# Optimization experiments

Hardware: AMD Instinct MI355X
Metric: run time of the kernel (lower is better)

## Reference

```python
import jax, jax.numpy as jnp
import numpy as np

HIDDEN = 1024
INTER = 256
N_EXPERTS = 16
B, T = 4, 2048
NEG_INF = -1000000000.0


def setup_inputs() -> dict:
    key = jax.random.key(0)
    ks = jax.random.split(key, 5)
    hidden_states = jax.random.normal(ks[0], (B, T, HIDDEN), dtype=jnp.float32)
    sim_matrix = jax.random.normal(ks[1], (HIDDEN, N_EXPERTS), dtype=jnp.float32)
    threshold = jnp.zeros((1,), dtype=jnp.float32)
    # torch Linear weights: w1 [I, C], w2 [C, I]; store per-expert stacked in
    # matmul-friendly layout: w1 [E, C, I], w2 [E, I, C]
    w1 = jax.random.normal(ks[2], (N_EXPERTS, HIDDEN, INTER), dtype=jnp.float32) / np.sqrt(HIDDEN)
    w2 = jax.random.normal(ks[3], (N_EXPERTS, INTER, HIDDEN), dtype=jnp.float32) / np.sqrt(INTER)
    return {"hidden_states": hidden_states, "sim_matrix": sim_matrix,
            "threshold": threshold, "w1": w1, "w2": w2}


def _l2norm(x, axis):
    return x / jnp.maximum(jnp.linalg.norm(x, axis=axis, keepdims=True), 1e-12)


def reference(hidden_states, sim_matrix, threshold, w1, w2):
    Bq, Tq, C = hidden_states.shape
    x = hidden_states.reshape(-1, C)                      # [N, C]
    # gate
    scores = _l2norm(x, -1) @ _l2norm(sim_matrix, 0)      # [N, E]
    activated = scores > threshold
    k_per_token = activated.sum(axis=-1)                  # [N] int
    masked = jnp.where(activated, scores, NEG_INF)
    routing_weights = jax.nn.softmax(masked, axis=-1)     # [N, E]
    # dense all-expert FFN
    h = jax.nn.gelu(jnp.einsum('nc,eci->nei', x, w1), approximate=False)
    out = jnp.einsum('nei,eic->nec', h, w2)               # [N, E, C]
    final = jnp.einsum('nec,ne->nc', out, routing_weights)
    return final.reshape(Bq, Tq, C), scores, k_per_token
```

## Files before the change

### kernel.cpp

```cpp
#include <hip/hip_runtime.h>
#include <hip/hip_bf16.h>
#include <math.h>

#define NTOK 8192
#define HID  1024
#define ISZ  256
#define NEXP 16
#define NBIG 4096

typedef __attribute__((ext_vector_type(8))) short bf16x8;
typedef __attribute__((ext_vector_type(4))) float f32x4;

__device__ __forceinline__ unsigned short f2bf(float f) {
  unsigned u = __float_as_uint(f);
  u += 0x7fff + ((u >> 16) & 1);
  return (unsigned short)(u >> 16);
}

__device__ __forceinline__ void async16(void* l, const void* g) {
  __builtin_amdgcn_global_load_lds(
      (const __attribute__((address_space(1))) unsigned int*)g,
      (__attribute__((address_space(3))) unsigned int*)l, 16, 0, 0);
}

__global__ void simnorm_kernel(const float* __restrict__ sm, float* __restrict__ inv_smn) {
  __shared__ float red[16][17];
  int t = threadIdx.x;
  int e = t & 15, g = t >> 4;
  float ss = 0.f;
  for (int c = g; c < HID; c += 16) {
    float v = sm[c * NEXP + e];
    ss += v * v;
  }
  red[e][g] = ss;
  __syncthreads();
  if (t < 16) {
    float s = 0.f;
    #pragma unroll
    for (int i = 0; i < 16; i++) s += red[t][i];
    inv_smn[t] = 1.f / fmaxf(sqrtf(s), 1e-12f);
  }
}

__global__ __launch_bounds__(256)
void gate_kernel(const float* __restrict__ x, const float* __restrict__ sm,
                 const float* __restrict__ thr, const float* __restrict__ inv_smn,
                 float* __restrict__ scores_out, float* __restrict__ k_out,
                 float* __restrict__ rw_out, unsigned short* __restrict__ xb_out) {
  const int n = blockIdx.x;
  const int t = threadIdx.x;
  const int lane = t & 63, wave = t >> 6;
  const float* xr = x + (size_t)n * HID;

  float p[16];
  #pragma unroll
  for (int e = 0; e < 16; e++) p[e] = 0.f;
  float ss = 0.f;

  #pragma unroll
  for (int q = 0; q < 4; q++) {
    int c = t + q * 256;
    float v = xr[c];
    ss += v * v;
    xb_out[(size_t)n * HID + c] = f2bf(v);
    const float4* smr = (const float4*)(sm + (size_t)c * NEXP);
    float4 s0 = smr[0], s1 = smr[1], s2 = smr[2], s3 = smr[3];
    p[0] += v * s0.x;  p[1] += v * s0.y;  p[2] += v * s0.z;  p[3] += v * s0.w;
    p[4] += v * s1.x;  p[5] += v * s1.y;  p[6] += v * s1.z;  p[7] += v * s1.w;
    p[8] += v * s2.x;  p[9] += v * s2.y;  p[10] += v * s2.z; p[11] += v * s2.w;
    p[12] += v * s3.x; p[13] += v * s3.y; p[14] += v * s3.z; p[15] += v * s3.w;
  }

  #pragma unroll
  for (int off = 32; off > 0; off >>= 1) {
    ss += __shfl_down(ss, off, 64);
    #pragma unroll
    for (int e = 0; e < 16; e++) p[e] += __shfl_down(p[e], off, 64);
  }

  __shared__ float red[4][17];
  __shared__ float sc[16];
  if (lane == 0) {
    red[wave][0] = ss;
    #pragma unroll
    for (int e = 0; e < 16; e++) red[wave][1 + e] = p[e];
  }
  __syncthreads();

  if (t < 16) {
    float d = red[0][1 + t] + red[1][1 + t] + red[2][1 + t] + red[3][1 + t];
    float ssum = red[0][0] + red[1][0] + red[2][0] + red[3][0];
    float inv_x = 1.f / fmaxf(sqrtf(ssum), 1e-12f);
    float s = d * inv_x * inv_smn[t];
    scores_out[(size_t)n * 16 + t] = s;
    sc[t] = s;
  }
  __syncthreads();

  if (t < 16) {
    float thrv = thr[0];
    float s = sc[t];
    bool act = s > thrv;
    float m = act ? s : -INFINITY;
    int cnt = act ? 1 : 0;
    #pragma unroll
    for (int off = 8; off > 0; off >>= 1) {
      m = fmaxf(m, __shfl_xor(m, off, 16));
      cnt += __shfl_xor(cnt, off, 16);
    }
    float pv;
    if (cnt > 0) pv = act ? expf(s - m) : 0.f;
    else         pv = 1.f;
    float sum = pv;
    #pragma unroll
    for (int off = 8; off > 0; off >>= 1) sum += __shfl_xor(sum, off, 16);
    rw_out[(size_t)n * 16 + t] = pv / sum;
    if (t == 0) k_out[n] = (float)cnt;
  }
}

__global__ __launch_bounds__(256)
void transpose_cast_kernel(const float* __restrict__ src, unsigned short* __restrict__ dst,
                           int R, int C, int dstride, int e_src_stride, int e_dst_mult) {
  __shared__ float tile[32][33];
  const int e = blockIdx.z;
  const int r0 = blockIdx.y * 32, c0 = blockIdx.x * 32;
  const int tx = threadIdx.x & 31, ty = threadIdx.x >> 5;
  const float* s = src + (size_t)e * e_src_stride;
  #pragma unroll
  for (int q = 0; q < 4; q++) {
    int r = r0 + ty + q * 8;
    tile[ty + q * 8][tx] = s[(size_t)r * C + c0 + tx];
  }
  __syncthreads();
  unsigned short* d = dst + (size_t)e * e_dst_mult;
  #pragma unroll
  for (int q = 0; q < 4; q++) {
    int cc = c0 + ty + q * 8;
    int r  = r0 + tx;
    d[(size_t)cc * dstride + r] = f2bf(tile[tx][ty + q * 8]);
  }
}

#define PHASE(QM, QN, SU, WAIT_)                                                      \
  {                                                                                   \
    bf16x8 afr[4][2], bfr[2][2];                                                      \
    _Pragma("unroll")                                                                 \
    for (int ml = 0; ml < 4; ml++) {                                                  \
      afr[ml][0] = *(const bf16x8*)(bufA + (QM)*16384 + wmo + ml*2048 + lro + colk0); \
      afr[ml][1] = *(const bf16x8*)(bufA + (QM)*16384 + wmo + ml*2048 + lro + colk1); \
    }                                                                                 \
    _Pragma("unroll")                                                                 \
    for (int nl = 0; nl < 2; nl++) {                                                  \
      bfr[nl][0] = *(const bf16x8*)(bufB + (QN)*16384 + wno + nl*2048 + lro + colk0); \
      bfr[nl][1] = *(const bf16x8*)(bufB + (QN)*16384 + wno + nl*2048 + lro + colk1); \
    }                                                                                 \
    _Pragma("unroll")                                                                 \
    for (int i = 0; i < 2; i++) {                                                     \
      if ((SU) == 0) async16(ldsAn + o16[i],         Ag + (size_t)aRow[i]*K + kn + aCol[i]);        \
      if ((SU) == 1) async16(ldsBn + o16[i],         Bg + (size_t)bRow[i]*K + kn + bCol[i]);        \
      if ((SU) == 2) async16(ldsAn + 16384 + o16[i], Ag + (size_t)(aRow[i] + 64)*K + kn + aCol[i]); \
      if ((SU) == 3) async16(ldsBn + 16384 + o16[i], Bg + (size_t)(bRow[i] + 32)*K + kn + bCol[i]); \
    }                                                                                 \
    __builtin_amdgcn_sched_barrier(0);                                                \
    __builtin_amdgcn_s_barrier();                                                     \
    asm volatile("s_waitcnt lgkmcnt(0)" ::: "memory");                                \
    __builtin_amdgcn_sched_barrier(0);                                                \
    __builtin_amdgcn_s_setprio(1);                                                    \
    _Pragma("unroll")                                                                 \
    for (int ml = 0; ml < 4; ml++)                                                    \
      _Pragma("unroll")                                                               \
      for (int nl = 0; nl < 2; nl++) {                                                \
        acc[(QM)*4+ml][(QN)*2+nl] = __builtin_amdgcn_mfma_f32_16x16x32_bf16(          \
            afr[ml][0], bfr[nl][0], acc[(QM)*4+ml][(QN)*2+nl], 0, 0, 0);              \
        acc[(QM)*4+ml][(QN)*2+nl] = __builtin_amdgcn_mfma_f32_16x16x32_bf16(          \
            afr[ml][1], bfr[nl][1], acc[(QM)*4+ml][(QN)*2+nl], 0, 0, 0);              \
      }                                                                               \
    __builtin_amdgcn_s_setprio(0);                                                    \
    __builtin_amdgcn_sched_barrier(0);                                                \
    if (WAIT_) { asm volatile("s_waitcnt vmcnt(4)" ::: "memory"); }                   \
    __builtin_amdgcn_s_barrier();                                                     \
  }

template <int EPI, int K, int NBN>
__global__ __launch_bounds__(512, 2)
void gemm256(const unsigned short* __restrict__ A, const unsigned short* __restrict__ B,
             float* __restrict__ Cf, unsigned short* __restrict__ Cb,
             const float* __restrict__ rw) {
  __shared__ __align__(1024) char lds[131072];
  constexpr int NT = K / 64;
  const int tid = threadIdx.x;
  const int lane = tid & 63, wid = tid >> 6;
  const int wm = wid >> 2, wn = wid & 3;
  const int lr = lane & 15;

  const int nwg = gridDim.x;
  const int cpx = nwg >> 3;
  const int wg = (blockIdx.x & 7) * cpx + (blockIdx.x >> 3);
  const int bm = wg / NBN, bn = wg % NBN;

  const int swz = (lr & 7) << 4;
  const int colk0 = ((lane >> 4) * 16) ^ swz;
  const int colk1 = (64 + (lane >> 4) * 16) ^ swz;
  const int wmo = wm * 8192, wno = wn * 4096, lro = lr * 128;

  int aRow[2], aCol[2], bRow[2], bCol[2], o16[2];
  #pragma unroll
  for (int i = 0; i < 2; i++) {
    int o = (i * 512 + tid) * 16;
    o16[i] = o;
    { int wmb = o >> 13, ob = o & 8191, r = ob >> 7, cb = ob & 127;
      aRow[i] = wmb * 128 + r; aCol[i] = (cb ^ ((r & 7) << 4)) >> 1; }
    { int wnb = o >> 12, ob = o & 4095, r = ob >> 7, cb = ob & 127;
      bRow[i] = wnb * 64 + r; bCol[i] = (cb ^ ((r & 7) << 4)) >> 1; }
  }

  const unsigned short* Ag = A + (size_t)bm * 256 * K;
  const unsigned short* Bg = B + (size_t)bn * 256 * K;

  f32x4 acc[8][4];
  #pragma unroll
  for (int m = 0; m < 8; m++)
    #pragma unroll
    for (int n = 0; n < 4; n++) acc[m][n] = (f32x4){0.f, 0.f, 0.f, 0.f};

  #pragma unroll
  for (int i = 0; i < 2; i++) async16(lds + o16[i],                 Ag + (size_t)aRow[i] * K + aCol[i]);
  #pragma unroll
  for (int i = 0; i < 2; i++) async16(lds + 65536 + o16[i],         Bg + (size_t)bRow[i] * K + bCol[i]);
  #pragma unroll
  for (int i = 0; i < 2; i++) async16(lds + 16384 + o16[i],         Ag + (size_t)(aRow[i] + 64) * K + aCol[i]);
  #pragma unroll
  for (int i = 0; i < 2; i++) async16(lds + 65536 + 16384 + o16[i], Bg + (size_t)(bRow[i] + 32) * K + bCol[i]);
  asm volatile("s_waitcnt vmcnt(0)" ::: "memory");
  __builtin_amdgcn_s_barrier();

  #pragma unroll 1
  for (int t = 0; t < NT; t += 2) {
    {
      const char* bufA = lds;
      const char* bufB = lds + 65536;
      char* ldsAn = lds + 32768;
      char* ldsBn = lds + 65536 + 32768;
      const int kn = ((t + 1) & (NT - 1)) << 6;
      PHASE(0, 0, 0, 1)
      PHASE(1, 0, 1, 1)
      PHASE(0, 1, 2, 0)
      PHASE(1, 1, 3, 1)
    }
    {
      const char* bufA = lds + 32768;
      const char* bufB = lds + 65536 + 32768;
      char* ldsAn = lds;
      char* ldsBn = lds + 65536;
      const int kn = ((t + 2) & (NT - 1)) << 6;
      PHASE(0, 0, 0, 1)
      PHASE(1, 0, 1, 1)
      PHASE(0, 1, 2, 0)
      PHASE(1, 1, 3, 1)
    }
  }

  asm volatile("s_waitcnt vmcnt(0)" ::: "memory");

  const int jr = (lane >> 4) * 4;
  if (EPI == 1) {
    float wrow[8][4];
    #pragma unroll
    for (int m = 0; m < 8; m++)
      #pragma unroll
      for (int j = 0; j < 4; j++)
        wrow[m][j] = rw[(size_t)(bm * 256 + wm * 128 + m * 16 + jr + j) * 16 + bn];
    #pragma unroll
    for (int m = 0; m < 8; m++) {
      #pragma unroll
      for (int n = 0; n < 4; n++) {
        int col = bn * 256 + wn * 64 + n * 16 + lr;
        #pragma unroll
        for (int j = 0; j < 4; j++) {
          int r = bm * 256 + wm * 128 + m * 16 + jr + j;
          float v = acc[m][n][j];
          float g = 0.7978845608f * (v + 0.044715f * v * v * v);
          float e = __expf(2.f * g);
          float th = 1.f - 2.f / (e + 1.f);
          float ge = 0.5f * v * (1.f + th);
          Cb[(size_t)r * NBIG + col] = f2bf(ge * wrow[m][j]);
        }
      }
    }
  } else {
    #pragma unroll
    for (int m = 0; m < 8; m++) {
      #pragma unroll
      for (int n = 0; n < 4; n++) {
        int col = bn * 256 + wn * 64 + n * 16 + lr;
        #pragma unroll
        for (int j = 0; j < 4; j++) {
          int r = bm * 256 + wm * 128 + m * 16 + jr + j;
          Cf[(size_t)r * HID + col] = acc[m][n][j];
        }
      }
    }
  }
}

extern "C" void kernel_launch(void* const* d_in, const int* in_sizes, int n_in,
                              void* d_out, int out_size, void* d_ws, size_t ws_size,
                              hipStream_t stream) {
  const float* x   = (const float*)d_in[0];
  const float* sm  = (const float*)d_in[1];
  const float* thr = (const float*)d_in[2];
  const float* w1  = (const float*)d_in[3];
  const float* w2  = (const float*)d_in[4];

  float* out_final  = (float*)d_out;
  float* out_scores = out_final + (size_t)NTOK * HID;
  float* out_k      = out_scores + (size_t)NTOK * NEXP;

  char* ws = (char*)d_ws;
  float* inv_smn = (float*)ws;
  float* rwbuf   = (float*)(ws + 256);
  unsigned short* Xb  = (unsigned short*)(ws + 256 + 524288);
  unsigned short* W1T = Xb + (size_t)NTOK * HID;
  unsigned short* W2T = W1T + (size_t)NBIG * HID;
  unsigned short* H   = W2T + (size_t)HID * NBIG;

  simnorm_kernel<<<1, 256, 0, stream>>>(sm, inv_smn);
  gate_kernel<<<NTOK, 256, 0, stream>>>(x, sm, thr, inv_smn, out_scores, out_k, rwbuf, Xb);
  transpose_cast_kernel<<<dim3(ISZ / 32, HID / 32, NEXP), 256, 0, stream>>>(
      w1, W1T, HID, ISZ, HID, HID * ISZ, ISZ * HID);
  transpose_cast_kernel<<<dim3(HID / 32, ISZ / 32, NEXP), 256, 0, stream>>>(
      w2, W2T, ISZ, HID, NBIG, ISZ * HID, ISZ);
  gemm256<1, HID, 16><<<512, 512, 0, stream>>>(Xb, W1T, nullptr, H, rwbuf);
  gemm256<2, NBIG, 4><<<128, 512, 0, stream>>>(H, W2T, out_final, nullptr, nullptr);
}
```

Baseline: 271.3 us.

## Split-K the second expert GEMM across two workgroup sets with reduction kernel

The down-projection GEMM (K=4096) originally launched only 128 workgroups. It now splits K in two, launching 256 workgroups. One half writes directly to the output and the other writes to a workspace buffer, and a new elementwise kernel adds the partials. This targets underutilisation of the device's compute units but costs an extra 32MB fp32 write/read pass and a launch. It falls back to the old path if the workspace is too small.

```diff
diff --git a/kernel.cpp b/kernel.cpp
--- a/kernel.cpp
+++ b/kernel.cpp
@@ -157,10 +157,10 @@
     }                                                                                 \
     _Pragma("unroll")                                                                 \
     for (int i = 0; i < 2; i++) {                                                     \
-      if ((SU) == 0) async16(ldsAn + o16[i],         Ag + (size_t)aRow[i]*K + kn + aCol[i]);        \
-      if ((SU) == 1) async16(ldsBn + o16[i],         Bg + (size_t)bRow[i]*K + kn + bCol[i]);        \
-      if ((SU) == 2) async16(ldsAn + 16384 + o16[i], Ag + (size_t)(aRow[i] + 64)*K + kn + aCol[i]); \
-      if ((SU) == 3) async16(ldsBn + 16384 + o16[i], Bg + (size_t)(bRow[i] + 32)*K + kn + bCol[i]); \
+      if ((SU) == 0) async16(ldsAn + o16[i],         Ag + (size_t)aRow[i]*LD + kn + aCol[i]);        \
+      if ((SU) == 1) async16(ldsBn + o16[i],         Bg + (size_t)bRow[i]*LD + kn + bCol[i]);        \
+      if ((SU) == 2) async16(ldsAn + 16384 + o16[i], Ag + (size_t)(aRow[i] + 64)*LD + kn + aCol[i]); \
+      if ((SU) == 3) async16(ldsBn + 16384 + o16[i], Bg + (size_t)(bRow[i] + 32)*LD + kn + bCol[i]); \
     }                                                                                 \
     __builtin_amdgcn_sched_barrier(0);                                                \
     __builtin_amdgcn_s_barrier();                                                     \
@@ -180,15 +180,16 @@
     __builtin_amdgcn_sched_barrier(0);                                                \
     if (WAIT_) { asm volatile("s_waitcnt vmcnt(4)" ::: "memory"); }                   \
     __builtin_amdgcn_s_barrier();                                                     \
-  }
-
-template <int EPI, int K, int NBN>
+    __builtin_amdgcn_sched_barrier(0);                                                \
+  }
+
+template <int EPI, int KEXT, int LD, int NBN, int SPLITK>
 __global__ __launch_bounds__(512, 2)
 void gemm256(const unsigned short* __restrict__ A, const unsigned short* __restrict__ B,
-             float* __restrict__ Cf, unsigned short* __restrict__ Cb,
-             const float* __restrict__ rw) {
+             float* __restrict__ Cf, float* __restrict__ Cf2,
+             unsigned short* __restrict__ Cb, const float* __restrict__ rw) {
   __shared__ __align__(1024) char lds[131072];
-  constexpr int NT = K / 64;
+  constexpr int NT = KEXT / 64;
   const int tid = threadIdx.x;
   const int lane = tid & 63, wid = tid >> 6;
   const int wm = wid >> 2, wn = wid & 3;
@@ -196,7 +197,9 @@
 
   const int nwg = gridDim.x;
   const int cpx = nwg >> 3;
-  const int wg = (blockIdx.x & 7) * cpx + (blockIdx.x >> 3);
+  int wg = (blockIdx.x & 7) * cpx + (blockIdx.x >> 3);
+  int kz = 0;
+  if (SPLITK == 2) { kz = wg / (nwg >> 1); wg = wg % (nwg >> 1); }
   const int bm = wg / NBN, bn = wg % NBN;
 
   const int swz = (lr & 7) << 4;
@@ -215,8 +218,8 @@
       bRow[i] = wnb * 64 + r; bCol[i] = (cb ^ ((r & 7) << 4)) >> 1; }
   }
 
-  const unsigned short* Ag = A + (size_t)bm * 256 * K;
-  const unsigned short* Bg = B + (size_t)bn * 256 * K;
+  const unsigned short* Ag = A + (size_t)bm * 256 * LD + (size_t)kz * KEXT;
+  const unsigned short* Bg = B + (size_t)bn * 256 * LD + (size_t)kz * KEXT;
 
   f32x4 acc[8][4];
   #pragma unroll
@@ -225,13 +228,13 @@
     for (int n = 0; n < 4; n++) acc[m][n] = (f32x4){0.f, 0.f, 0.f, 0.f};
 
   #pragma unroll
-  for (int i = 0; i < 2; i++) async16(lds + o16[i],                 Ag + (size_t)aRow[i] * K + aCol[i]);
-  #pragma unroll
-  for (int i = 0; i < 2; i++) async16(lds + 65536 + o16[i],         Bg + (size_t)bRow[i] * K + bCol[i]);
-  #pragma unroll
-  for (int i = 0; i < 2; i++) async16(lds + 16384 + o16[i],         Ag + (size_t)(aRow[i] + 64) * K + aCol[i]);
-  #pragma unroll
-  for (int i = 0; i < 2; i++) async16(lds + 65536 + 16384 + o16[i], Bg + (size_t)(bRow[i] + 32) * K + bCol[i]);
+  for (int i = 0; i < 2; i++) async16(lds + o16[i],                 Ag + (size_t)aRow[i] * LD + aCol[i]);
+  #pragma unroll
+  for (int i = 0; i < 2; i++) async16(lds + 65536 + o16[i],         Bg + (size_t)bRow[i] * LD + bCol[i]);
+  #pragma unroll
+  for (int i = 0; i < 2; i++) async16(lds + 16384 + o16[i],         Ag + (size_t)(aRow[i] + 64) * LD + aCol[i]);
+  #pragma unroll
+  for (int i = 0; i < 2; i++) async16(lds + 65536 + 16384 + o16[i], Bg + (size_t)(bRow[i] + 32) * LD + bCol[i]);
   asm volatile("s_waitcnt vmcnt(0)" ::: "memory");
   __builtin_amdgcn_s_barrier();
 
@@ -289,6 +292,7 @@
       }
     }
   } else {
+    float* cfp = (SPLITK == 2 && kz == 1) ? Cf2 : Cf;
     #pragma unroll
     for (int m = 0; m < 8; m++) {
       #pragma unroll
@@ -297,10 +301,22 @@
         #pragma unroll
         for (int j = 0; j < 4; j++) {
           int r = bm * 256 + wm * 128 + m * 16 + jr + j;
-          Cf[(size_t)r * HID + col] = acc[m][n][j];
+          cfp[(size_t)r * HID + col] = acc[m][n][j];
         }
       }
     }
+  }
+}
+
+__global__ __launch_bounds__(256)
+void addk(float* __restrict__ out, const float* __restrict__ p1, int n4) {
+  int i = blockIdx.x * blockDim.x + threadIdx.x;
+  const int stride = gridDim.x * blockDim.x;
+  for (; i < n4; i += stride) {
+    float4 a = ((const float4*)out)[i];
+    float4 b = ((const float4*)p1)[i];
+    a.x += b.x; a.y += b.y; a.z += b.z; a.w += b.w;
+    ((float4*)out)[i] = a;
   }
 }
 
@@ -318,12 +334,15 @@
   float* out_k      = out_scores + (size_t)NTOK * NEXP;
 
   char* ws = (char*)d_ws;
-  float* inv_smn = (float*)ws;
-  float* rwbuf   = (float*)(ws + 256);
-  unsigned short* Xb  = (unsigned short*)(ws + 256 + 524288);
-  unsigned short* W1T = Xb + (size_t)NTOK * HID;
-  unsigned short* W2T = W1T + (size_t)NBIG * HID;
-  unsigned short* H   = W2T + (size_t)HID * NBIG;
+  size_t off = 0;
+  float* inv_smn = (float*)(ws + off); off += 256;
+  float* rwbuf   = (float*)(ws + off); off += (size_t)NTOK * NEXP * 4;
+  unsigned short* Xb  = (unsigned short*)(ws + off); off += (size_t)NTOK * HID * 2;
+  unsigned short* W1T = (unsigned short*)(ws + off); off += (size_t)NBIG * HID * 2;
+  unsigned short* W2T = (unsigned short*)(ws + off); off += (size_t)HID * NBIG * 2;
+  unsigned short* H   = (unsigned short*)(ws + off); off += (size_t)NTOK * NBIG * 2;
+  float* P1 = (float*)(ws + off);
+  const bool split = ws_size >= off + (size_t)NTOK * HID * 4;
 
   simnorm_kernel<<<1, 256, 0, stream>>>(sm, inv_smn);
   gate_kernel<<<NTOK, 256, 0, stream>>>(x, sm, thr, inv_smn, out_scores, out_k, rwbuf, Xb);
@@ -331,6 +350,13 @@
       w1, W1T, HID, ISZ, HID, HID * ISZ, ISZ * HID);
   transpose_cast_kernel<<<dim3(HID / 32, ISZ / 32, NEXP), 256, 0, stream>>>(
       w2, W2T, ISZ, HID, NBIG, ISZ * HID, ISZ);
-  gemm256<1, HID, 16><<<512, 512, 0, stream>>>(Xb, W1T, nullptr, H, rwbuf);
-  gemm256<2, NBIG, 4><<<128, 512, 0, stream>>>(H, W2T, out_final, nullptr, nullptr);
-}
+
+  gemm256<1, HID, HID, 16, 1><<<512, 512, 0, stream>>>(Xb, W1T, nullptr, nullptr, H, rwbuf);
+
+  if (split) {
+    gemm256<2, NBIG / 2, NBIG, 4, 2><<<256, 512, 0, stream>>>(H, W2T, out_final, P1, nullptr, nullptr);
+    addk<<<2048, 256, 0, stream>>>(out_final, P1, NTOK * HID / 4);
+  } else {
+    gemm256<2, NBIG, NBIG, 4, 1><<<128, 512, 0, stream>>>(H, W2T, out_final, nullptr, nullptr, nullptr);
+  }
+}
```

Result: faster. 242.5 us (-10.6%).
